# Performance work log

Measured on AMD Instinct MI355X. Metric: run time of the kernel, lower is better.

## Reference

```python
import math
import jax, jax.numpy as jnp
import numpy as np

HEADS = 8


def setup_inputs() -> dict:
    key = jax.random.key(0)
    k1, k2 = jax.random.split(key)
    b, heads, c, t, s_enc = 4, HEADS, 64, 1024, 1024
    x = jax.random.normal(k1, (b, 3 * heads * c, t), dtype=jnp.float32)
    encoder_kv = jax.random.normal(k2, (b, 2 * heads * c, s_enc), dtype=jnp.float32)
    return {"x": x, "encoder_kv": encoder_kv}


def reference(x, encoder_kv):
    heads = HEADS
    b, ch3, t = x.shape
    c = ch3 // (3 * heads)
    s_enc = encoder_kv.shape[-1]
    # 'b (qkv heads c) h -> qkv (b heads) c h'
    qkv = x.reshape(b, 3, heads, c, t).transpose(1, 0, 2, 3, 4).reshape(3, b * heads, c, t)
    q, k, v = qkv[0], qkv[1], qkv[2]
    ekv = encoder_kv.reshape(b, 2, heads, c, s_enc).transpose(1, 0, 2, 3, 4).reshape(2, b * heads, c, s_enc)
    ek, ev = ekv[0], ekv[1]
    k = jnp.concatenate([ek, k], axis=-1)  # (bh, c, s_enc + t)
    v = jnp.concatenate([ev, v], axis=-1)
    scale = 1.0 / math.sqrt(math.sqrt(c))
    weight = jnp.einsum('bct,bcs->bts', q * scale, k * scale)  # (bh, t, s)
    weight = jax.nn.softmax(weight.astype(jnp.float32), axis=-1).astype(weight.dtype)
    out = jnp.einsum('bts,bcs->bct', weight, v)  # (bh, c, t)
    # '(b heads) c h -> b (heads c) h'
    out = out.reshape(b, heads, c, t).reshape(b, heads * c, t)
    return out
```

## Files before the change

### kernel.cpp

```cpp
#include <hip/hip_runtime.h>

typedef __attribute__((ext_vector_type(8))) short bf16x8;
typedef __attribute__((ext_vector_type(16))) float f32x16;
typedef __attribute__((ext_vector_type(4))) unsigned int u32x4;

#define NH 8
#define CD 64
#define TLEN 1024
#define SENC 1024
#define STOT 2048
#define SK 64
#define NIT (STOT / SK)
#define BQ 64
#define QSCALE 0.18033688f

__device__ __forceinline__ ushort f2bf(float f) {
  uint x = __builtin_bit_cast(uint, f);
  uint r = (x + 0x7fffu + ((x >> 16) & 1u)) >> 16;
  return (ushort)r;
}
__device__ __forceinline__ uint4 pack8(const ushort* p) {
  uint4 u;
  u.x = (uint)p[0] | ((uint)p[1] << 16);
  u.y = (uint)p[2] | ((uint)p[3] << 16);
  u.z = (uint)p[4] | ((uint)p[5] << 16);
  u.w = (uint)p[6] | ((uint)p[7] << 16);
  return u;
}
__device__ __forceinline__ uint cvtpk(float lo, float hi) {
  uint r;
  asm("v_cvt_pk_bf16_f32 %0, %1, %2" : "=v"(r) : "v"(lo), "v"(hi));
  return r;
}
__device__ __forceinline__ void plswap(uint& a, uint& b) {
  asm("v_permlane32_swap_b32 %0, %1" : "+v"(a), "+v"(b));
}
__device__ __forceinline__ bf16x8 mk8(uint a, uint b, uint c, uint d) {
  u32x4 t = {a, b, c, d};
  return __builtin_bit_cast(bf16x8, t);
}

__global__ __launch_bounds__(256)
void repack_kernel(const float* __restrict__ x, const float* __restrict__ ekv,
                   ushort* __restrict__ ktw, ushort* __restrict__ vnw) {
  const int kx = blockIdx.x;
  const int bh = blockIdx.y;
  const int b = bh >> 3, h = bh & 7;
  const int t = threadIdx.x;
  const float* ks;
  const float* vs;
  if (kx < 16) {
    ks = ekv + (size_t)(b * 2 * NH * CD + h * CD) * SENC + kx * 64;
    vs = ekv + (size_t)(b * 2 * NH * CD + NH * CD + h * CD) * SENC + kx * 64;
  } else {
    ks = x + (size_t)(b * 3 * NH * CD + NH * CD + h * CD) * TLEN + (kx - 16) * 64;
    vs = x + (size_t)(b * 3 * NH * CD + 2 * NH * CD + h * CD) * TLEN + (kx - 16) * 64;
  }
  if (blockIdx.z == 0) {
    __shared__ float Lt[64 * 65];
    const int ci = t >> 2, seg = t & 3;
#pragma unroll
    for (int j = 0; j < 4; ++j) {
      float4 d = *(const float4*)&ks[ci * 1024 + seg * 16 + 4 * j];
      Lt[ci * 65 + seg * 16 + 4 * j + 0] = d.x;
      Lt[ci * 65 + seg * 16 + 4 * j + 1] = d.y;
      Lt[ci * 65 + seg * 16 + 4 * j + 2] = d.z;
      Lt[ci * 65 + seg * 16 + 4 * j + 3] = d.w;
    }
    __syncthreads();
    const int key = t >> 2;
    ushort tmp[16];
#pragma unroll
    for (int u = 0; u < 16; ++u)
      tmp[u] = f2bf(Lt[(seg * 16 + u) * 65 + key]);
    ushort* dst = ktw + ((size_t)bh * STOT + kx * 64 + key) * CD + seg * 16;
    *(uint4*)dst = pack8(tmp);
    *(uint4*)(dst + 8) = pack8(tmp + 8);
  } else {
    const int ci = t >> 2, seg = t & 3;
    ushort tmp[16];
#pragma unroll
    for (int j = 0; j < 4; ++j) {
      float4 d = *(const float4*)&vs[ci * 1024 + seg * 16 + 4 * j];
      tmp[4 * j + 0] = f2bf(d.x);
      tmp[4 * j + 1] = f2bf(d.y);
      tmp[4 * j + 2] = f2bf(d.z);
      tmp[4 * j + 3] = f2bf(d.w);
    }
    ushort* dst = vnw + (size_t)bh * CD * STOT + (size_t)ci * STOT + kx * 64 + seg * 16;
    *(uint4*)dst = pack8(tmp);
    *(uint4*)(dst + 8) = pack8(tmp + 8);
  }
}

__global__ __launch_bounds__(128, 2)
void qkv_attn_ws(const float* __restrict__ x, const ushort* __restrict__ ktw,
                 const ushort* __restrict__ vnw, float* __restrict__ out) {
  __shared__ __align__(16) ushort Kb[2][SK * CD];
  __shared__ __align__(16) ushort Vb[2][CD * SK];

  const int tid  = threadIdx.x;
  const int w    = tid >> 6;
  const int lane = tid & 63;
  const int al   = lane & 31;
  const int h    = lane >> 5;
  const int xm   = lane & 7;

  const int f  = blockIdx.x;
  const int bh = (f & 7) | ((f >> 7) << 3);
  const int qt = (f >> 3) & 15;
  const int b  = bh >> 3;
  const int hh = bh & 7;
  const int t0 = qt * BQ;

  const float* qg = x + (size_t)(b * 3 * NH * CD + hh * CD) * TLEN;
  float* og = out + (size_t)(b * NH * CD + hh * CD) * TLEN;
  const ushort* ktb = ktw + (size_t)bh * STOT * CD;
  const ushort* vnb = vnw + (size_t)bh * CD * STOT;

  const int srow = tid >> 1;
  const int cb   = (tid & 1) * 4;
  int swz[4];
#pragma unroll
  for (int j = 0; j < 4; ++j) swz[j] = (((cb + j) ^ (srow & 7)) * 8);

  uint4 kp[4], vp[4];
#pragma unroll
  for (int j = 0; j < 4; ++j) {
    kp[j] = *(const uint4*)(ktb + (size_t)srow * CD + (cb + j) * 8);
    vp[j] = *(const uint4*)(vnb + (size_t)srow * STOT + (cb + j) * 8);
  }
#pragma unroll
  for (int j = 0; j < 4; ++j) {
    *(uint4*)&Kb[0][srow * CD + swz[j]] = kp[j];
    *(uint4*)&Vb[0][srow * CD + swz[j]] = vp[j];
  }

  const int q_l = w * 32 + al;
  const float* qp = qg + t0 + q_l;
  float qv[4][8];
#pragma unroll
  for (int kst = 0; kst < 4; ++kst)
#pragma unroll
    for (int j = 0; j < 8; ++j)
      qv[kst][j] = qp[(size_t)(kst * 16 + h * 8 + j) * TLEN] * QSCALE;
  bf16x8 qfrag[4];
#pragma unroll
  for (int kst = 0; kst < 4; ++kst)
    qfrag[kst] = mk8(cvtpk(qv[kst][0], qv[kst][1]), cvtpk(qv[kst][2], qv[kst][3]),
                     cvtpk(qv[kst][4], qv[kst][5]), cvtpk(qv[kst][6], qv[kst][7]));

  __syncthreads();

  int koff[4];
#pragma unroll
  for (int kst = 0; kst < 4; ++kst) koff[kst] = ((2 * kst + h) ^ xm) * 8;

  f32x16 of0, of1;
#pragma unroll
  for (int i = 0; i < 16; ++i) { of0[i] = 0.f; of1[i] = 0.f; }
  float l_acc = 0.f;

  for (int it = 0; it < NIT; ++it) {
    const int cur = it & 1;

    if (it + 1 < NIT) {
      const int s1 = (it + 1) * SK;
#pragma unroll
      for (int j = 0; j < 4; ++j) {
        kp[j] = *(const uint4*)(ktb + (size_t)(s1 + srow) * CD + (cb + j) * 8);
        vp[j] = *(const uint4*)(vnb + (size_t)srow * STOT + s1 + (cb + j) * 8);
      }
    }

    const ushort* kt = Kb[cur];
    const ushort* vt = Vb[cur];

    uint ulo[8], uhi[8];
#pragma unroll
    for (int mt = 0; mt < 2; ++mt) {
      f32x16 acc;
#pragma unroll
      for (int i = 0; i < 16; ++i) acc[i] = 0.f;
#pragma unroll
      for (int kst = 0; kst < 4; ++kst) {
        bf16x8 afr = *(const bf16x8*)&kt[(mt * 32 + al) * CD + koff[kst]];
        acc = __builtin_amdgcn_mfma_f32_32x32x16_bf16(afr, qfrag[kst], acc, 0, 0, 0);
      }
#pragma unroll
      for (int rq = 0; rq < 4; ++rq) {
        float p0 = exp2f(acc[4 * rq + 0]);
        float p1 = exp2f(acc[4 * rq + 1]);
        float p2 = exp2f(acc[4 * rq + 2]);
        float p3 = exp2f(acc[4 * rq + 3]);
        l_acc += (p0 + p1) + (p2 + p3);
        ulo[4 * mt + rq] = cvtpk(p0, p1);
        uhi[4 * mt + rq] = cvtpk(p2, p3);
      }
    }

    bf16x8 pfr[4];
#pragma unroll
    for (int kst = 0; kst < 4; ++kst) {
      uint xlo = ulo[2 * kst], ylo = ulo[2 * kst + 1];
      uint xhi = uhi[2 * kst], yhi = uhi[2 * kst + 1];
      plswap(xlo, ylo);
      plswap(xhi, yhi);
      pfr[kst] = mk8(xlo, xhi, ylo, yhi);
    }

#pragma unroll
    for (int kst = 0; kst < 4; ++kst) {
      bf16x8 v0 = *(const bf16x8*)&vt[(0 * 32 + al) * CD + koff[kst]];
      bf16x8 v1 = *(const bf16x8*)&vt[(1 * 32 + al) * CD + koff[kst]];
      of0 = __builtin_amdgcn_mfma_f32_32x32x16_bf16(v0, pfr[kst], of0, 0, 0, 0);
      of1 = __builtin_amdgcn_mfma_f32_32x32x16_bf16(v1, pfr[kst], of1, 0, 0, 0);
    }

    if (it + 1 < NIT) {
      const int nb = cur ^ 1;
#pragma unroll
      for (int j = 0; j < 4; ++j) {
        *(uint4*)&Kb[nb][srow * CD + swz[j]] = kp[j];
        *(uint4*)&Vb[nb][srow * CD + swz[j]] = vp[j];
      }
      __syncthreads();
    }
  }

  {
    float lv = l_acc + __shfl_xor(l_acc, 32);
    float inv = 1.0f / lv;
    float* ob = og + t0 + q_l;
#pragma unroll
    for (int r = 0; r < 16; ++r) {
      int ci = (r & 3) + 8 * (r >> 2) + 4 * h;
      ob[(size_t)ci * TLEN] = of0[r] * inv;
      ob[(size_t)(32 + ci) * TLEN] = of1[r] * inv;
    }
  }
}

extern "C" void kernel_launch(void* const* d_in, const int* in_sizes, int n_in,
                              void* d_out, int out_size, void* d_ws, size_t ws_size,
                              hipStream_t stream) {
  const float* x   = (const float*)d_in[0];
  const float* ekv = (const float*)d_in[1];
  float* out = (float*)d_out;
  ushort* ktw = (ushort*)d_ws;
  ushort* vnw = ktw + (size_t)32 * STOT * CD;
  repack_kernel<<<dim3(32, 32, 2), 256, 0, stream>>>(x, ekv, ktw, vnw);
  qkv_attn_ws<<<512, 128, 0, stream>>>(x, ktw, vnw, out);
}
```

Baseline: 131.7 us.

## Split attention keys across two blocks and combine partial outputs in a separate kernel

The key range is split into two halves, so the attention grid doubles from 512 to 1024 blocks. Each block writes its unnormalized partial output and partial softmax denominator to workspace. A new combine kernel then sums the two partials and divides by the summed denominators. This is meant to raise CU occupancy and latency hiding on a grid that previously gave only about two blocks per CU. The cost is extra global traffic for the partials, plus one more kernel launch.

After: 120.6 us. 8.5% less time.

```diff
diff --git a/kernel.cpp b/kernel.cpp
--- a/kernel.cpp
+++ b/kernel.cpp
@@ -2,6 +2,7 @@
 
 typedef __attribute__((ext_vector_type(8))) short bf16x8;
 typedef __attribute__((ext_vector_type(16))) float f32x16;
+typedef __attribute__((ext_vector_type(4))) float f32x4;
 typedef __attribute__((ext_vector_type(4))) unsigned int u32x4;
 
 #define NH 8
@@ -10,7 +11,9 @@
 #define SENC 1024
 #define STOT 2048
 #define SK 64
-#define NIT (STOT / SK)
+#define NSPLIT 2
+#define SKEYS (STOT / NSPLIT)
+#define NITS (SKEYS / SK)
 #define BQ 64
 #define QSCALE 0.18033688f
 
@@ -95,7 +98,8 @@
 
 __global__ __launch_bounds__(128, 2)
 void qkv_attn_ws(const float* __restrict__ x, const ushort* __restrict__ ktw,
-                 const ushort* __restrict__ vnw, float* __restrict__ out) {
+                 const ushort* __restrict__ vnw, float* __restrict__ po,
+                 float* __restrict__ lw) {
   __shared__ __align__(16) ushort Kb[2][SK * CD];
   __shared__ __align__(16) ushort Vb[2][CD * SK];
 
@@ -107,16 +111,19 @@
   const int xm   = lane & 7;
 
   const int f  = blockIdx.x;
-  const int bh = (f & 7) | ((f >> 7) << 3);
+  const int bh = (f & 7) | (((f >> 8) & 3) << 3);
   const int qt = (f >> 3) & 15;
+  const int ks = (f >> 7) & 1;
   const int b  = bh >> 3;
   const int hh = bh & 7;
   const int t0 = qt * BQ;
+  const int kbase = ks * SKEYS;
 
   const float* qg = x + (size_t)(b * 3 * NH * CD + hh * CD) * TLEN;
-  float* og = out + (size_t)(b * NH * CD + hh * CD) * TLEN;
   const ushort* ktb = ktw + (size_t)bh * STOT * CD;
   const ushort* vnb = vnw + (size_t)bh * CD * STOT;
+  float* pob = po + ((size_t)ks * 32 + bh) * CD * TLEN;
+  float* lwb = lw + ((size_t)ks * 32 + bh) * TLEN;
 
   const int srow = tid >> 1;
   const int cb   = (tid & 1) * 4;
@@ -127,8 +134,8 @@
   uint4 kp[4], vp[4];
 #pragma unroll
   for (int j = 0; j < 4; ++j) {
-    kp[j] = *(const uint4*)(ktb + (size_t)srow * CD + (cb + j) * 8);
-    vp[j] = *(const uint4*)(vnb + (size_t)srow * STOT + (cb + j) * 8);
+    kp[j] = *(const uint4*)(ktb + (size_t)(kbase + srow) * CD + (cb + j) * 8);
+    vp[j] = *(const uint4*)(vnb + (size_t)srow * STOT + kbase + (cb + j) * 8);
   }
 #pragma unroll
   for (int j = 0; j < 4; ++j) {
@@ -161,11 +168,11 @@
   for (int i = 0; i < 16; ++i) { of0[i] = 0.f; of1[i] = 0.f; }
   float l_acc = 0.f;
 
-  for (int it = 0; it < NIT; ++it) {
+  for (int it = 0; it < NITS; ++it) {
     const int cur = it & 1;
 
-    if (it + 1 < NIT) {
-      const int s1 = (it + 1) * SK;
+    if (it + 1 < NITS) {
+      const int s1 = kbase + (it + 1) * SK;
 #pragma unroll
       for (int j = 0; j < 4; ++j) {
         kp[j] = *(const uint4*)(ktb + (size_t)(s1 + srow) * CD + (cb + j) * 8);
@@ -217,7 +224,7 @@
       of1 = __builtin_amdgcn_mfma_f32_32x32x16_bf16(v1, pfr[kst], of1, 0, 0, 0);
     }
 
-    if (it + 1 < NIT) {
+    if (it + 1 < NITS) {
       const int nb = cur ^ 1;
 #pragma unroll
       for (int j = 0; j < 4; ++j) {
@@ -230,15 +237,38 @@
 
   {
     float lv = l_acc + __shfl_xor(l_acc, 32);
-    float inv = 1.0f / lv;
-    float* ob = og + t0 + q_l;
+    float* ob = pob + t0 + q_l;
 #pragma unroll
     for (int r = 0; r < 16; ++r) {
       int ci = (r & 3) + 8 * (r >> 2) + 4 * h;
-      ob[(size_t)ci * TLEN] = of0[r] * inv;
-      ob[(size_t)(32 + ci) * TLEN] = of1[r] * inv;
-    }
-  }
+      ob[(size_t)ci * TLEN] = of0[r];
+      ob[(size_t)(32 + ci) * TLEN] = of1[r];
+    }
+    if (h == 0) lwb[t0 + q_l] = lv;
+  }
+}
+
+__global__ __launch_bounds__(256)
+void combine_kernel(const float* __restrict__ po, const float* __restrict__ lw,
+                    float* __restrict__ out) {
+  const int idx = blockIdx.x * 256 + threadIdx.x;
+  const int row = idx >> 7;
+  const int t8  = (idx & 127) * 8;
+  const int bh  = row >> 6;
+  const size_t KSS = (size_t)32 * CD * TLEN;
+  const float* p0 = po + (size_t)row * TLEN + t8;
+  const float* p1 = p0 + KSS;
+  const float* l0 = lw + (size_t)bh * TLEN + t8;
+  const float* l1 = l0 + (size_t)32 * TLEN;
+  f32x4 a0 = *(const f32x4*)p0,       a1 = *(const f32x4*)(p0 + 4);
+  f32x4 b0 = *(const f32x4*)p1,       b1 = *(const f32x4*)(p1 + 4);
+  f32x4 u0 = *(const f32x4*)l0,       u1 = *(const f32x4*)(l0 + 4);
+  f32x4 v0 = *(const f32x4*)l1,       v1 = *(const f32x4*)(l1 + 4);
+  f32x4 r0 = (a0 + b0) / (u0 + v0);
+  f32x4 r1 = (a1 + b1) / (u1 + v1);
+  float* o = out + (size_t)row * TLEN + t8;
+  *(f32x4*)o = r0;
+  *(f32x4*)(o + 4) = r1;
 }
 
 extern "C" void kernel_launch(void* const* d_in, const int* in_sizes, int n_in,
@@ -249,6 +279,9 @@
   float* out = (float*)d_out;
   ushort* ktw = (ushort*)d_ws;
   ushort* vnw = ktw + (size_t)32 * STOT * CD;
+  float*  po  = (float*)(vnw + (size_t)32 * STOT * CD);
+  float*  lw  = po + (size_t)NSPLIT * 32 * CD * TLEN;
   repack_kernel<<<dim3(32, 32, 2), 256, 0, stream>>>(x, ekv, ktw, vnw);
-  qkv_attn_ws<<<512, 128, 0, stream>>>(x, ktw, vnw, out);
-}
+  qkv_attn_ws<<<32 * 16 * NSPLIT, 128, 0, stream>>>(x, ktw, vnw, po, lw);
+  combine_kernel<<<1024, 256, 0, stream>>>(po, lw, out);
+}
```
